# Optimization experiments

Hardware: AMD Instinct MI355X
Metric: run time of the kernel (lower is better)

Reference implementation:

```python
import jax, jax.numpy as jnp
import numpy as np

B, T, D, U = 32, 2048, 512, 512


def setup_inputs() -> dict:
    key = jax.random.key(0)
    ks = jax.random.split(key, 6)
    scale = 0.05
    return {
        "values": jax.random.normal(ks[0], (B, T, D), dtype=jnp.float32),
        "query": jax.random.normal(ks[1], (B, D), dtype=jnp.float32),
        "W1_w": jax.random.normal(ks[2], (D, U), dtype=jnp.float32) * scale,
        "W1_b": jnp.zeros((U,), dtype=jnp.float32),
        "W2_w": jax.random.normal(ks[3], (D, U), dtype=jnp.float32) * scale,
        "W2_b": jnp.zeros((U,), dtype=jnp.float32),
        "V_w": jax.random.normal(ks[4], (U, 1), dtype=jnp.float32) * scale,
        "V_b": jnp.zeros((1,), dtype=jnp.float32),
    }


def reference(values, query, W1_w, W1_b, W2_w, W2_b, V_w, V_b):
    # values: [B, T, D]; query: [B, D]
    proj_v = jnp.einsum("btd,du->btu", values, W1_w) + W1_b          # [B, T, U]
    proj_q = (query @ W2_w + W2_b)[:, None, :]                        # [B, 1, U]
    score = jnp.tanh(proj_v + proj_q) @ V_w + V_b                     # [B, T, 1]
    attention_weights = jax.nn.softmax(score, axis=1)                 # [B, T, 1]
    context_vector = jnp.sum(attention_weights * values, axis=1)      # [B, D]
    return context_vector, attention_weights
```

## Files before the change

kernel.cpp:

```cpp
#include <hip/hip_runtime.h>
#include <hip/hip_bf16.h>
#include <stdint.h>


#define B_DIM 32
#define T_DIM 2048
#define D_DIM 512
#define U_DIM 512
#define M_DIM (B_DIM * T_DIM)

typedef short bf16x8 __attribute__((ext_vector_type(8)));
typedef float f32x4 __attribute__((ext_vector_type(4)));

__device__ __forceinline__ float fast_tanh(float x) {
    float e = __expf(2.0f * x);
    return 1.0f - __fdividef(2.0f, e + 1.0f);
}

__device__ __forceinline__ short bf16r(float x) {
    unsigned u = __float_as_uint(x);
    u += 0x7fffu + ((u >> 16) & 1u);
    return (short)(u >> 16);
}

__device__ __forceinline__ bf16x8 pack8v(f32x4 a, f32x4 b) {
    union { __hip_bfloat162 h[4]; bf16x8 v; } u;
    u.h[0] = __float22bfloat162_rn(make_float2(a[0], a[1]));
    u.h[1] = __float22bfloat162_rn(make_float2(a[2], a[3]));
    u.h[2] = __float22bfloat162_rn(make_float2(b[0], b[1]));
    u.h[3] = __float22bfloat162_rn(make_float2(b[2], b[3]));
    return u.v;
}

__device__ __forceinline__ void g2lds16(const void* g, void* lds) {
    auto gp = reinterpret_cast<const __attribute__((address_space(1))) unsigned int*>(
        reinterpret_cast<uintptr_t>(g));
    auto lp = reinterpret_cast<__attribute__((address_space(3))) unsigned int*>(
        (unsigned int)(uintptr_t)lds);
    __builtin_amdgcn_global_load_lds(gp, lp, 16, 0, 0);
}


__global__ void prep_kernel(const float* __restrict__ W1_w,
                            const float* __restrict__ W1_b,
                            const float* __restrict__ W2_w,
                            const float* __restrict__ W2_b,
                            const float* __restrict__ query,
                            unsigned short* __restrict__ W1T,
                            float* __restrict__ qb) {
    __shared__ float red[256];
    const int tid = threadIdx.x;
    if (blockIdx.x < 128) {
        int n = blockIdx.x * 256 + tid;
        int uu    = n & 255;
        int kc    = (n >> 8) & 3;
        int kstep = (n >> 10) & 15;
        int ut    = n >> 14;
        int u  = ut * 256 + uu;
        int k0 = kstep * 32 + kc * 8;
        bf16x8 pk;
#pragma unroll
        for (int j = 0; j < 8; ++j)
            pk[j] = bf16r(W1_w[(size_t)(k0 + j) * U_DIM + u]);
        ((bf16x8*)W1T)[n] = pk;
    } else {
        int bid = blockIdx.x - 128;
        int b  = bid >> 3;
        int ug = bid & 7;
        int u  = ug * 64 + (tid & 63);
        int dq = tid >> 6;
        const float* q  = query + b * D_DIM + dq * 128;
        const float* w2 = W2_w + (size_t)(dq * 128) * U_DIM + u;
        float acc = 0.f;
#pragma unroll 8
        for (int d = 0; d < 128; ++d)
            acc += q[d] * w2[(size_t)d * U_DIM];
        red[tid] = acc;
        __syncthreads();
        if (tid < 64) {
            qb[b * U_DIM + u] = red[tid] + red[tid + 64] + red[tid + 128]
                              + red[tid + 192] + W2_b[u] + W1_b[u];
        }
    }
}

__global__ __launch_bounds__(256, 4) void score_kernel(
        const float* __restrict__ values,
        const unsigned short* __restrict__ W1T,
        const float* __restrict__ qb,
        const float* __restrict__ Vw,
        float* __restrict__ sP) {
    __shared__ __align__(16) unsigned char smem[2][16384];

    const int tid  = threadIdx.x;
    const int lane = tid & 63;
    const int w    = tid >> 6;
    const int l15  = lane & 15;
    const int quad = lane >> 4;
    const int wr   = w >> 1;
    const int wc   = w & 1;
    const int ut   = blockIdx.x & 1;
    const int mb   = (blockIdx.x >> 1) * 64;
    const int b    = mb >> 11;

    const float* arow0 = values + (size_t)(mb + wr * 32 + l15) * D_DIM + quad * 8;
    const float* arow1 = arow0 + 16 * D_DIM;
    const unsigned short* wsrc = W1T + (size_t)ut * 16 * 8192;
    unsigned char* sm0 = &smem[0][0];
    const unsigned char* bb = sm0 + (size_t)(quad * 256 + wc * 128 + l15) * 16;

#pragma unroll
    for (int i = 0; i < 4; ++i) {
        int unit = i * 256 + tid;
        g2lds16(wsrc + (size_t)unit * 8, sm0 + unit * 16);
    }

    f32x4 acc[2][8] = {};

    for (int ks = 0; ks < 16; ++ks) {
        f32x4 a00 = *(const f32x4*)(arow0 + ks * 32);
        f32x4 a01 = *(const f32x4*)(arow0 + ks * 32 + 4);
        f32x4 a10 = *(const f32x4*)(arow1 + ks * 32);
        f32x4 a11 = *(const f32x4*)(arow1 + ks * 32 + 4);

        __syncthreads();

        if (ks < 15) {
            const unsigned short* src = wsrc + (size_t)(ks + 1) * 8192;
            unsigned char* nbuf = sm0 + ((ks + 1) & 1) * 16384;
#pragma unroll
            for (int i = 0; i < 4; ++i) {
                int unit = i * 256 + tid;
                g2lds16(src + (size_t)unit * 8, nbuf + unit * 16);
            }
        }

        bf16x8 a0 = pack8v(a00, a01);
        bf16x8 a1 = pack8v(a10, a11);
        const unsigned char* bbk = bb + (ks & 1) * 16384;
        __builtin_amdgcn_s_setprio(1);
#pragma unroll
        for (int ui = 0; ui < 8; ++ui) {
            bf16x8 bf = *(const bf16x8*)(bbk + ui * 256);
            acc[0][ui] = __builtin_amdgcn_mfma_f32_16x16x32_bf16(a0, bf, acc[0][ui], 0, 0, 0);
            acc[1][ui] = __builtin_amdgcn_mfma_f32_16x16x32_bf16(a1, bf, acc[1][ui], 0, 0, 0);
        }
        __builtin_amdgcn_s_setprio(0);
    }

    const int ub = ut * 256 + wc * 128 + l15;
    float sm[2][4] = {};
#pragma unroll
    for (int ui = 0; ui < 8; ++ui) {
        const int u = ub + ui * 16;
        const float qv = qb[b * U_DIM + u];
        const float vw = Vw[u];
#pragma unroll
        for (int mt = 0; mt < 2; ++mt)
#pragma unroll
            for (int r = 0; r < 4; ++r)
                sm[mt][r] += fast_tanh(acc[mt][ui][r] + qv) * vw;
    }
#pragma unroll
    for (int mt = 0; mt < 2; ++mt)
#pragma unroll
        for (int r = 0; r < 4; ++r) {
            float v = sm[mt][r];
            v += __shfl_xor(v, 1, 64);
            v += __shfl_xor(v, 2, 64);
            v += __shfl_xor(v, 4, 64);
            v += __shfl_xor(v, 8, 64);
            sm[mt][r] = v;
        }
    if (l15 == 0) {
        const int slice = ut * 2 + wc;
#pragma unroll
        for (int mt = 0; mt < 2; ++mt)
#pragma unroll
            for (int r = 0; r < 4; ++r)
                sP[(size_t)slice * M_DIM + mb + wr * 32 + mt * 16 + quad * 4 + r] = sm[mt][r];
    }
}

__global__ void softmax_kernel(const float* __restrict__ sP,
                               float* __restrict__ out) {
    const int b = blockIdx.x;
    const int tid = threadIdx.x;

    float v[8];
    float mx = -1e30f;
#pragma unroll
    for (int i = 0; i < 8; ++i) {
        int m = b * T_DIM + i * 256 + tid;
        v[i] = sP[m] + sP[M_DIM + m] + sP[2 * M_DIM + m] + sP[3 * M_DIM + m];
        mx = fmaxf(mx, v[i]);
    }
#pragma unroll
    for (int off = 1; off < 64; off <<= 1)
        mx = fmaxf(mx, __shfl_xor(mx, off, 64));
    __shared__ float redm[4];
    if ((tid & 63) == 0) redm[tid >> 6] = mx;
    __syncthreads();
    mx = fmaxf(fmaxf(redm[0], redm[1]), fmaxf(redm[2], redm[3]));

    float sum = 0.f;
#pragma unroll
    for (int i = 0; i < 8; ++i) {
        v[i] = __expf(v[i] - mx);
        sum += v[i];
    }
#pragma unroll
    for (int off = 1; off < 64; off <<= 1)
        sum += __shfl_xor(sum, off, 64);
    __shared__ float reds[4];
    if ((tid & 63) == 0) reds[tid >> 6] = sum;
    __syncthreads();
    sum = reds[0] + reds[1] + reds[2] + reds[3];

    const float inv = 1.0f / sum;
#pragma unroll
    for (int i = 0; i < 8; ++i)
        out[B_DIM * D_DIM + b * T_DIM + i * 256 + tid] = v[i] * inv;
}

__global__ void context_kernel(const float* __restrict__ values,
                               const float* __restrict__ weights,
                               float* __restrict__ P) {
    __shared__ float sw[64];
    __shared__ float red[512];
    const int tc = blockIdx.x;
    const int b  = blockIdx.y;
    const int tid = threadIdx.x;
    const int d4 = tid & 127;
    const int th = tid >> 7;

    if (tid < 64) sw[tid] = weights[b * T_DIM + tc * 64 + tid];
    __syncthreads();

    const float4* vb = (const float4*)(values + ((size_t)b * T_DIM + tc * 64) * D_DIM) + d4;
    float4 acc = {0.f, 0.f, 0.f, 0.f};
#pragma unroll 8
    for (int i = th; i < 64; i += 2) {
        float wv = sw[i];
        float4 vv = vb[(size_t)i * 128];
        acc.x += wv * vv.x; acc.y += wv * vv.y;
        acc.z += wv * vv.z; acc.w += wv * vv.w;
    }
    if (th == 1) ((float4*)red)[d4] = acc;
    __syncthreads();
    if (th == 0) {
        float4 o = ((float4*)red)[d4];
        acc.x += o.x; acc.y += o.y; acc.z += o.z; acc.w += o.w;
        *(float4*)(P + ((size_t)(b * 32 + tc)) * 512 + d4 * 4) = acc;
    }
}

__global__ void reduce_kernel(const float* __restrict__ P,
                              float* __restrict__ ctx) {
    const int g = blockIdx.x * 256 + threadIdx.x;
    const int b = g >> 9, d = g & 511;
    float s = 0.f;
#pragma unroll
    for (int tc = 0; tc < 32; ++tc)
        s += P[((size_t)(b * 32 + tc)) * 512 + d];
    ctx[g] = s;
}

extern "C" void kernel_launch(void* const* d_in, const int* in_sizes, int n_in,
                              void* d_out, int out_size, void* d_ws, size_t ws_size,
                              hipStream_t stream) {
    const float* values = (const float*)d_in[0];
    const float* query  = (const float*)d_in[1];
    const float* W1_w   = (const float*)d_in[2];
    const float* W1_b   = (const float*)d_in[3];
    const float* W2_w   = (const float*)d_in[4];
    const float* W2_b   = (const float*)d_in[5];
    const float* V_w    = (const float*)d_in[6];

    float* out = (float*)d_out;

    unsigned char* ws = (unsigned char*)d_ws;
    unsigned short* W1T = (unsigned short*)(ws);
    float* qb = (float*)(ws + 524288);
    float* sP = (float*)(ws + 524288 + 65536);
    float* P  = (float*)(ws + 524288 + 65536 + 1048576);

    prep_kernel<<<384, 256, 0, stream>>>(W1_w, W1_b, W2_w, W2_b, query, W1T, qb);
    score_kernel<<<2048, 256, 0, stream>>>(values, W1T, qb, V_w, sP);
    softmax_kernel<<<B_DIM, 256, 0, stream>>>(sP, out);
    context_kernel<<<dim3(32, B_DIM), 256, 0, stream>>>(values, out + B_DIM * D_DIM, P);
    reduce_kernel<<<64, 256, 0, stream>>>(P, out);
}
```

Baseline: 291.0 us.

## Load W1 fragments directly from global into registers, dropping LDS staging

The score kernel no longer stages W1T tiles through a double-buffered LDS via global_load_lds with per-step __syncthreads. Each lane now loads its eight bf16x8 B fragments straight from global memory (L2/L1-cached) each k-step, and the k loop is no longer unrolled. This removes the block barriers and the LDS footprint, which may allow higher occupancy. In exchange, each wave issues redundant global loads that other waves in the block also make, and there is no software prefetch, so load latency is exposed unless occupancy hides it.

```diff
diff --git a/kernel.cpp b/kernel.cpp
--- a/kernel.cpp
+++ b/kernel.cpp
@@ -30,14 +30,6 @@
     u.h[2] = __float22bfloat162_rn(make_float2(b[0], b[1]));
     u.h[3] = __float22bfloat162_rn(make_float2(b[2], b[3]));
     return u.v;
-}
-
-__device__ __forceinline__ void g2lds16(const void* g, void* lds) {
-    auto gp = reinterpret_cast<const __attribute__((address_space(1))) unsigned int*>(
-        reinterpret_cast<uintptr_t>(g));
-    auto lp = reinterpret_cast<__attribute__((address_space(3))) unsigned int*>(
-        (unsigned int)(uintptr_t)lds);
-    __builtin_amdgcn_global_load_lds(gp, lp, 16, 0, 0);
 }
 
 
@@ -90,8 +82,6 @@
         const float* __restrict__ qb,
         const float* __restrict__ Vw,
         float* __restrict__ sP) {
-    __shared__ __align__(16) unsigned char smem[2][16384];
-
     const int tid  = threadIdx.x;
     const int lane = tid & 63;
     const int w    = tid >> 6;
@@ -105,45 +95,31 @@
 
     const float* arow0 = values + (size_t)(mb + wr * 32 + l15) * D_DIM + quad * 8;
     const float* arow1 = arow0 + 16 * D_DIM;
-    const unsigned short* wsrc = W1T + (size_t)ut * 16 * 8192;
-    unsigned char* sm0 = &smem[0][0];
-    const unsigned char* bb = sm0 + (size_t)(quad * 256 + wc * 128 + l15) * 16;
-
-#pragma unroll
-    for (int i = 0; i < 4; ++i) {
-        int unit = i * 256 + tid;
-        g2lds16(wsrc + (size_t)unit * 8, sm0 + unit * 16);
-    }
+    const unsigned short* bbase =
+        W1T + ((size_t)ut * 16384 + quad * 256 + wc * 128 + l15) * 8;
 
     f32x4 acc[2][8] = {};
 
+#pragma unroll 1
     for (int ks = 0; ks < 16; ++ks) {
+        const unsigned short* bks = bbase + (size_t)ks * 8192;
+        bf16x8 bfr[8];
+#pragma unroll
+        for (int ui = 0; ui < 8; ++ui)
+            bfr[ui] = *(const bf16x8*)(bks + (size_t)ui * 128);
+
         f32x4 a00 = *(const f32x4*)(arow0 + ks * 32);
         f32x4 a01 = *(const f32x4*)(arow0 + ks * 32 + 4);
         f32x4 a10 = *(const f32x4*)(arow1 + ks * 32);
         f32x4 a11 = *(const f32x4*)(arow1 + ks * 32 + 4);
 
-        __syncthreads();
-
-        if (ks < 15) {
-            const unsigned short* src = wsrc + (size_t)(ks + 1) * 8192;
-            unsigned char* nbuf = sm0 + ((ks + 1) & 1) * 16384;
-#pragma unroll
-            for (int i = 0; i < 4; ++i) {
-                int unit = i * 256 + tid;
-                g2lds16(src + (size_t)unit * 8, nbuf + unit * 16);
-            }
-        }
-
         bf16x8 a0 = pack8v(a00, a01);
         bf16x8 a1 = pack8v(a10, a11);
-        const unsigned char* bbk = bb + (ks & 1) * 16384;
         __builtin_amdgcn_s_setprio(1);
 #pragma unroll
         for (int ui = 0; ui < 8; ++ui) {
-            bf16x8 bf = *(const bf16x8*)(bbk + ui * 256);
-            acc[0][ui] = __builtin_amdgcn_mfma_f32_16x16x32_bf16(a0, bf, acc[0][ui], 0, 0, 0);
-            acc[1][ui] = __builtin_amdgcn_mfma_f32_16x16x32_bf16(a1, bf, acc[1][ui], 0, 0, 0);
+            acc[0][ui] = __builtin_amdgcn_mfma_f32_16x16x32_bf16(a0, bfr[ui], acc[0][ui], 0, 0, 0);
+            acc[1][ui] = __builtin_amdgcn_mfma_f32_16x16x32_bf16(a1, bfr[ui], acc[1][ui], 0, 0, 0);
         }
         __builtin_amdgcn_s_setprio(0);
     }
```

New measurement: 303.8 us. +4.4%, slower.
